# Kernel optimization log

Hardware: AMD Instinct MI355X
Metric: run time of the kernel (lower is better)

The kernel has to match this reference:

```python
import jax, jax.numpy as jnp
import numpy as np

IN_DIM = 128
OUT_DIM = 128
NUM_HEADS = 8
HEAD_DIM = OUT_DIM // NUM_HEADS  # 16
FFN_DIM = OUT_DIM * 2
LN_EPS = 1e-5


def _layer_norm(x, g, b):
    mu = jnp.mean(x, axis=-1, keepdims=True)
    var = jnp.var(x, axis=-1, keepdims=True)
    return (x - mu) * jax.lax.rsqrt(var + LN_EPS) * g + b


def setup_inputs() -> dict:
    key = jax.random.key(0)
    ks = jax.random.split(key, 12)
    B, N = 4, 2048
    s_in = 1.0 / np.sqrt(IN_DIM)
    s_out = 1.0 / np.sqrt(OUT_DIM)
    s_ffn = 1.0 / np.sqrt(FFN_DIM)
    return {
        "adj_matrix": jax.random.randint(ks[0], (N, N), 0, 2, dtype=jnp.int32),
        "h": jax.random.normal(ks[1], (B, N, IN_DIM), dtype=jnp.float32),
        # Q/K/V: Linear(in_dim, out_dim) with use_bias=False, stored as [in, out]
        "Wq": jax.random.uniform(ks[2], (IN_DIM, OUT_DIM), jnp.float32, -s_in, s_in),
        "Wk": jax.random.uniform(ks[3], (IN_DIM, OUT_DIM), jnp.float32, -s_in, s_in),
        "Wv": jax.random.uniform(ks[4], (IN_DIM, OUT_DIM), jnp.float32, -s_in, s_in),
        "Wo": jax.random.uniform(ks[5], (OUT_DIM, OUT_DIM), jnp.float32, -s_out, s_out),
        "bo": jnp.zeros((OUT_DIM,), jnp.float32),
        "ln1_g": jnp.ones((OUT_DIM,), jnp.float32),
        "ln1_b": jnp.zeros((OUT_DIM,), jnp.float32),
        "W1": jax.random.uniform(ks[6], (OUT_DIM, FFN_DIM), jnp.float32, -s_out, s_out),
        "b1": jnp.zeros((FFN_DIM,), jnp.float32),
        "W2": jax.random.uniform(ks[7], (FFN_DIM, OUT_DIM), jnp.float32, -s_ffn, s_ffn),
        "b2": jnp.zeros((OUT_DIM,), jnp.float32),
        "ln2_g": jnp.ones((OUT_DIM,), jnp.float32),
        "ln2_b": jnp.zeros((OUT_DIM,), jnp.float32),
    }


def reference(adj_matrix, h, Wq, Wk, Wv, Wo, bo, ln1_g, ln1_b,
              W1, b1, W2, b2, ln2_g, ln2_b):
    B, N, _ = h.shape
    # QKV projections -> [B, N, H, D]
    Q = (h @ Wq).reshape(B, N, NUM_HEADS, HEAD_DIM)
    K = (h @ Wk).reshape(B, N, NUM_HEADS, HEAD_DIM)
    V = (h @ Wv).reshape(B, N, NUM_HEADS, HEAD_DIM)
    scores = jnp.einsum('bnhd,bmhd->bhnm', Q, K) / jnp.sqrt(
        jnp.asarray(HEAD_DIM, jnp.float32))
    # adjacency-masked attention: mask broadcast over batch and heads
    mask = (adj_matrix == 0)[None, None, :, :]  # [1,1,N,N]
    scores = jnp.where(mask, -jnp.inf, scores)
    attn = jax.nn.softmax(scores, axis=-1)
    attn_out = jnp.einsum('bhnm,bmhd->bnhd', attn, V).reshape(B, N, OUT_DIM)
    # output projection + residual + LN
    x = h + (attn_out @ Wo + bo)
    x = _layer_norm(x, ln1_g, ln1_b)
    # FFN + residual + LN
    y = jax.nn.relu(x @ W1 + b1) @ W2 + b2
    x = _layer_norm(x + y, ln2_g, ln2_b)
    return x
```

## Files before the change

kernel.cpp:

```cpp
#include <hip/hip_runtime.h>

#define B_   4
#define N_   2048
#define DIM  128
#define NH   8
#define HD   16
#define FFN_ 256
#define LN_EPS 1e-5f
#define BN   (B_*N_)
#define LOG2E 1.44269504f

#if __has_builtin(__builtin_amdgcn_exp2f)
#define EXP2(x) __builtin_amdgcn_exp2f(x)
#else
#define EXP2(x) exp2f(x)
#endif

typedef __bf16 bf16x8 __attribute__((ext_vector_type(8)));
typedef short  s16x8  __attribute__((ext_vector_type(8)));
typedef float  f32x16 __attribute__((ext_vector_type(16)));
typedef unsigned int u32x4 __attribute__((ext_vector_type(4)));

template<class T> struct as_short_vec { using type = s16x8; };

template <class T>
__device__ auto mfma_try(T a, T b, f32x16 c, int)
    -> decltype(__builtin_amdgcn_mfma_f32_32x32x16_bf16(a, b, c, 0, 0, 0)) {
  return __builtin_amdgcn_mfma_f32_32x32x16_bf16(a, b, c, 0, 0, 0);
}
template <class T>
__device__ f32x16 mfma_try(T a, T b, f32x16 c, long) {
  return __builtin_amdgcn_mfma_f32_32x32x16_bf16(
      __builtin_bit_cast(typename as_short_vec<T>::type, a),
      __builtin_bit_cast(typename as_short_vec<T>::type, b), c, 0, 0, 0);
}
__device__ __forceinline__ f32x16 mfma_bf(bf16x8 a, bf16x8 b, f32x16 c) {
  return mfma_try(a, b, c, 0);
}

__global__ __launch_bounds__(256) void k_prep(
    const int* __restrict__ adj,
    const float* __restrict__ W1, const float* __restrict__ W2,
    const float* __restrict__ Wq, const float* __restrict__ Wk,
    const float* __restrict__ Wv, const float* __restrict__ Wo,
    unsigned int* __restrict__ adjbT,
    __bf16* __restrict__ W1t, __bf16* __restrict__ W2t,
    __bf16* __restrict__ Wqt, __bf16* __restrict__ Wkt,
    __bf16* __restrict__ Wvt, __bf16* __restrict__ Wot,
    __bf16* __restrict__ onesb) {
    const int blk = blockIdx.x;
    const int tid = threadIdx.x;
    if (blk < 16384) {
        long long idx = (long long)blk * 256 + tid;
        int v = adj[idx] != 0;
        unsigned long long m = __ballot(v);
        if ((tid & 63) == 0) {
            int q  = (int)(idx >> 11);
            int kc = ((int)idx & 2047) >> 5;
            adjbT[(size_t)kc * 2048 + q]       = (unsigned)m;
            adjbT[(size_t)(kc + 1) * 2048 + q] = (unsigned)(m >> 32);
        }
    } else {
        const int g = (blk - 16384) * 256 + tid;
        {
            int k = g >> 8, n = g & 255;
            W1t[(size_t)n * 128 + k] = (__bf16)W1[(size_t)k * 256 + n];
        }
        {
            int k = g >> 7, n = g & 127;
            W2t[(size_t)n * 256 + k] = (__bf16)W2[(size_t)k * 128 + n];
        }
        if (g < 16384) {
            int k = g >> 7, n = g & 127;
            size_t s = (size_t)k * 128 + n, d = (size_t)n * 128 + k;
            Wqt[d] = (__bf16)(Wq[s] * (0.25f * LOG2E));
            Wkt[d] = (__bf16)Wk[s];
            Wvt[d] = (__bf16)Wv[s];
            Wot[d] = (__bf16)Wo[s];
        }
        if (g < 2080) onesb[g] = (__bf16)1.0f;
    }
}

__global__ __launch_bounds__(256) void k_qkv(
    const float* __restrict__ h,
    const __bf16* __restrict__ Wqt, const __bf16* __restrict__ Wkt,
    const __bf16* __restrict__ Wvt,
    __bf16* __restrict__ Qb, __bf16* __restrict__ Kb, __bf16* __restrict__ Vt) {
    const int r0   = blockIdx.x * 32;
    const int tid  = threadIdx.x;
    const int w    = tid >> 6;
    const int lane = tid & 63;
    const int l31  = lane & 31, hi = lane >> 5;

    __shared__ __bf16 Hs[32 * 128];

    for (int i = tid; i < 512; i += 256) {
        int row = i >> 4, u = i & 15;
        const float* src = h + (size_t)(r0 + row) * DIM + u * 8;
        float4 f0 = *(const float4*)src, f1 = *(const float4*)(src + 4);
        bf16x8 v;
        v[0] = (__bf16)f0.x; v[1] = (__bf16)f0.y; v[2] = (__bf16)f0.z; v[3] = (__bf16)f0.w;
        v[4] = (__bf16)f1.x; v[5] = (__bf16)f1.y; v[6] = (__bf16)f1.z; v[7] = (__bf16)f1.w;
        int byte = (row * 256 + u * 16) ^ ((row & 7) << 4);
        *(bf16x8*)((char*)Hs + byte) = v;
    }
    __syncthreads();

    f32x16 aq, ak, av;
    #pragma unroll
    for (int i = 0; i < 16; ++i) { aq[i] = 0.f; ak[i] = 0.f; av[i] = 0.f; }
    #pragma unroll
    for (int kk = 0; kk < 8; ++kk) {
        int byte = (l31 * 256 + kk * 32 + hi * 16) ^ ((l31 & 7) << 4);
        bf16x8 a = *(const bf16x8*)((const char*)Hs + byte);
        const size_t wo = (size_t)(w * 32 + l31) * 128 + kk * 16 + hi * 8;
        aq = mfma_bf(a, *(const bf16x8*)(Wqt + wo), aq);
        ak = mfma_bf(a, *(const bf16x8*)(Wkt + wo), ak);
        av = mfma_bf(a, *(const bf16x8*)(Wvt + wo), av);
    }
    const int n  = w * 32 + l31;
    const int hh = n >> 4, d = n & 15;
    const int b  = r0 >> 11;
    const size_t qbase = (size_t)(b * NH + hh) * N_;
    const size_t vbase = ((size_t)(b * NH + hh) * HD + d) * N_;
    #pragma unroll
    for (int r = 0; r < 16; ++r) {
        int mm   = (r & 3) + 8 * (r >> 2) + 4 * hi;
        int nloc = (r0 & (N_ - 1)) + mm;
        size_t qk = (qbase + nloc) * HD + d;
        Qb[qk] = (__bf16)aq[r];
        Kb[qk] = (__bf16)ak[r];
        int gg = (nloc >> 2) & 7;
        int ng = (gg & 4) | ((gg & 1) << 1) | ((gg >> 1) & 1);
        Vt[vbase + ((nloc & ~31) | (ng << 2) | (nloc & 3))] = (__bf16)av[r];
    }
}

__global__ __launch_bounds__(512, 4) void k_attn(
    const __bf16* __restrict__ Qb, const __bf16* __restrict__ Kb,
    const __bf16* __restrict__ Vt, const unsigned int* __restrict__ adjbT,
    const __bf16* __restrict__ onesb,
    __bf16* __restrict__ AOb) {
    const int bid  = (blockIdx.x & 7) * 256 + (blockIdx.x >> 3);
    const int qt   = bid & 63;
    const int hh   = (bid >> 6) & 7;
    const int b    = bid >> 9;
    const int kq   = threadIdx.x >> 6;
    const int lane = threadIdx.x & 63;
    const int l31  = lane & 31, hi = lane >> 5;
    const int q     = qt * 32 + l31;
    const int kbase = kq * 256;
    const int NT    = 8;

    __shared__ float accL[7][64][9];
    __shared__ uint2 lutM[16];

    if (threadIdx.x < 16) {
        unsigned v = threadIdx.x;
        lutM[v].x = ((v & 1u) ? 0xFFFFu : 0u) | ((v & 2u) ? 0xFFFF0000u : 0u);
        lutM[v].y = ((v & 4u) ? 0xFFFFu : 0u) | ((v & 8u) ? 0xFFFF0000u : 0u);
    }
    __syncthreads();

    const __bf16* Qh = Qb + (size_t)(b * NH + hh) * N_ * HD;
    const __bf16* Kp = Kb + (size_t)(b * NH + hh) * N_ * HD
                          + (size_t)(kbase + l31) * HD + hi * 8;
    const __bf16* Vp = ((l31 < 16)
        ? (Vt + ((size_t)(b * NH + hh) * HD + l31) * N_)
        : onesb) + kbase + hi * 8;
    const unsigned int* wp = adjbT + (size_t)(kq * NT) * 2048 + q;

    bf16x8 qf = *(const bf16x8*)(Qh + (size_t)q * HD + hi * 8);

    f32x16 acc;
    #pragma unroll
    for (int i = 0; i < 16; ++i) acc[i] = 0.f;
    const f32x16 z = {};

    bf16x8 kf  = *(const bf16x8*)Kp;
    bf16x8 vfa = *(const bf16x8*)Vp;
    bf16x8 vfb = *(const bf16x8*)(Vp + 16);
    unsigned int w32 = wp[0];

    #pragma unroll
    for (int t = 0; t < NT; ++t) {
        bf16x8 kf_n = {}, vfa_n = {}, vfb_n = {};
        unsigned int w32_n = 0;
        if (t + 1 < NT) {
            kf_n  = *(const bf16x8*)(Kp + (t + 1) * 32 * HD);
            vfa_n = *(const bf16x8*)(Vp + (t + 1) * 32);
            vfb_n = *(const bf16x8*)(Vp + (t + 1) * 32 + 16);
            w32_n = wp[(size_t)(t + 1) * 2048];
        }

        const unsigned ws = w32 >> (4 * hi);
        uint2 e0 = lutM[ws & 15u];
        uint2 e1 = lutM[(ws >> 8) & 15u];
        uint2 e2 = lutM[(ws >> 16) & 15u];
        uint2 e3 = lutM[(ws >> 24) & 15u];

        f32x16 st = mfma_bf(kf, qf, z);

        float p[16];
        #pragma unroll
        for (int r = 0; r < 16; ++r) p[r] = EXP2(st[r]);
        bf16x8 pa, pb;
        #pragma unroll
        for (int r = 0; r < 8; ++r) { pa[r] = (__bf16)p[r]; pb[r] = (__bf16)p[r + 8]; }

        u32x4 mA = {e0.x, e0.y, e1.x, e1.y};
        u32x4 mB = {e2.x, e2.y, e3.x, e3.y};
        pa = __builtin_bit_cast(bf16x8, __builtin_bit_cast(u32x4, pa) & mA);
        pb = __builtin_bit_cast(bf16x8, __builtin_bit_cast(u32x4, pb) & mB);

        acc = mfma_bf(vfa, pa, acc);
        acc = mfma_bf(vfb, pb, acc);

        if (t + 1 < NT) { kf = kf_n; vfa = vfa_n; vfb = vfb_n; w32 = w32_n; }
    }

    if (kq != 0) {
        #pragma unroll
        for (int r = 0; r < 9; ++r) accL[kq - 1][lane][r] = acc[r];
    }
    __syncthreads();
    if (kq == 0) {
        float tot[9];
        #pragma unroll
        for (int r = 0; r < 9; ++r) {
            float v = acc[r];
            #pragma unroll
            for (int i = 0; i < 7; ++i) v += accL[i][lane][r];
            tot[r] = v;
        }
        float inv = 1.f / tot[8];
        bf16x8 ov;
        #pragma unroll
        for (int r = 0; r < 8; ++r) ov[r] = (__bf16)(tot[r] * inv);
        u32x4 ou = __builtin_bit_cast(u32x4, ov);
        __bf16* op = AOb + ((size_t)(b * N_ + q)) * DIM + hh * HD + 4 * hi;
        uint2 w0 = { ou[0], ou[1] }, w1 = { ou[2], ou[3] };
        *(uint2*)op       = w0;
        *(uint2*)(op + 8) = w1;
    }
}

__global__ __launch_bounds__(256) void k_tail(
    const __bf16* __restrict__ AOb, const float* __restrict__ h,
    const __bf16* __restrict__ Wot, const float* __restrict__ bo,
    const float* __restrict__ g1, const float* __restrict__ b1ln,
    const __bf16* __restrict__ W1t, const float* __restrict__ b1,
    const __bf16* __restrict__ W2t, const float* __restrict__ b2,
    const float* __restrict__ g2, const float* __restrict__ b2ln,
    float* __restrict__ out) {
    const int r0   = blockIdx.x * 32;
    const int tid  = threadIdx.x;
    const int w    = tid >> 6;
    const int lane = tid & 63;
    const int l31  = lane & 31, hi = lane >> 5;

    __shared__ __bf16 As[32 * 128];
    __shared__ __bf16 Xs[32 * 128];
    __shared__ __bf16 Ts[32 * 256];
    __shared__ float  vv[32][DIM];

    for (int i = tid; i < 512; i += 256) {
        int row = i >> 4, u = i & 15;
        bf16x8 v = *(const bf16x8*)(AOb + (size_t)(r0 + row) * DIM + u * 8);
        int byte = (row * 256 + u * 16) ^ ((row & 7) << 4);
        *(bf16x8*)((char*)As + byte) = v;
    }
    __syncthreads();

    f32x16 acc;
    #pragma unroll
    for (int i = 0; i < 16; ++i) acc[i] = 0.f;
    #pragma unroll
    for (int kk = 0; kk < 8; ++kk) {
        int byte = (l31 * 256 + kk * 32 + hi * 16) ^ ((l31 & 7) << 4);
        bf16x8 a = *(const bf16x8*)((const char*)As + byte);
        acc = mfma_bf(a, *(const bf16x8*)(Wot + (size_t)(w * 32 + l31) * 128 + kk * 16 + hi * 8), acc);
    }
    {
        int n = w * 32 + l31;
        float bb = bo[n];
        #pragma unroll
        for (int r = 0; r < 16; ++r) {
            int mm = (r & 3) + 8 * (r >> 2) + 4 * hi;
            vv[mm][n] = acc[r] + bb + h[(size_t)(r0 + mm) * DIM + n];
        }
    }
    __syncthreads();

    {
        const int ln = lane;
        float gc0 = g1[ln], bc0 = b1ln[ln], gc1 = g1[ln + 64], bc1 = b1ln[ln + 64];
        #pragma unroll
        for (int i = 0; i < 8; ++i) {
            int rr = w * 8 + i;
            float x0 = vv[rr][ln], x1 = vv[rr][ln + 64];
            float s = x0 + x1, s2 = x0 * x0 + x1 * x1;
            for (int off = 1; off < 64; off <<= 1) {
                s  += __shfl_xor(s,  off);
                s2 += __shfl_xor(s2, off);
            }
            float mu  = s * (1.f / DIM);
            float var = s2 * (1.f / DIM) - mu * mu;
            float rs  = rsqrtf(var + LN_EPS);
            int byte0 = (rr * 256 + ln * 2) ^ ((rr & 7) << 4);
            int byte1 = (rr * 256 + (ln + 64) * 2) ^ ((rr & 7) << 4);
            *(__bf16*)((char*)Xs + byte0) = (__bf16)((x0 - mu) * rs * gc0 + bc0);
            *(__bf16*)((char*)Xs + byte1) = (__bf16)((x1 - mu) * rs * gc1 + bc1);
        }
    }
    __syncthreads();

    f32x16 acc1a, acc1b;
    #pragma unroll
    for (int i = 0; i < 16; ++i) { acc1a[i] = 0.f; acc1b[i] = 0.f; }
    #pragma unroll
    for (int kk = 0; kk < 8; ++kk) {
        int byte = (l31 * 256 + kk * 32 + hi * 16) ^ ((l31 & 7) << 4);
        bf16x8 a = *(const bf16x8*)((const char*)Xs + byte);
        bf16x8 bA = *(const bf16x8*)(W1t + (size_t)(w * 32 + l31) * 128 + kk * 16 + hi * 8);
        bf16x8 bB = *(const bf16x8*)(W1t + (size_t)((w + 4) * 32 + l31) * 128 + kk * 16 + hi * 8);
        acc1a = mfma_bf(a, bA, acc1a);
        acc1b = mfma_bf(a, bB, acc1b);
    }
    #pragma unroll
    for (int ct = 0; ct < 2; ++ct) {
        const f32x16& ac = ct ? acc1b : acc1a;
        int n = (w + ct * 4) * 32 + l31;
        float bb = b1[n];
        #pragma unroll
        for (int r = 0; r < 16; ++r) {
            int mm = (r & 3) + 8 * (r >> 2) + 4 * hi;
            float v = fmaxf(ac[r] + bb, 0.f);
            int byte = (mm * 512 + n * 2) ^ ((mm & 7) << 4);
            *(__bf16*)((char*)Ts + byte) = (__bf16)v;
        }
    }
    __syncthreads();

    f32x16 acc2;
    #pragma unroll
    for (int i = 0; i < 16; ++i) acc2[i] = 0.f;
    #pragma unroll
    for (int kk = 0; kk < 16; ++kk) {
        int byte = (l31 * 512 + kk * 32 + hi * 16) ^ ((l31 & 7) << 4);
        bf16x8 a = *(const bf16x8*)((const char*)Ts + byte);
        bf16x8 bb = *(const bf16x8*)(W2t + (size_t)(w * 32 + l31) * 256 + kk * 16 + hi * 8);
        acc2 = mfma_bf(a, bb, acc2);
    }
    {
        int n = w * 32 + l31;
        float bb = b2[n];
        #pragma unroll
        for (int r = 0; r < 16; ++r) {
            int mm = (r & 3) + 8 * (r >> 2) + 4 * hi;
            int byteR = (mm * 256 + n * 2) ^ ((mm & 7) << 4);
            float resid = (float)*(const __bf16*)((const char*)Xs + byteR);
            vv[mm][n] = acc2[r] + bb + resid;
        }
    }
    __syncthreads();

    {
        const int ln = lane;
        float gc0 = g2[ln], bc0 = b2ln[ln], gc1 = g2[ln + 64], bc1 = b2ln[ln + 64];
        #pragma unroll
        for (int i = 0; i < 8; ++i) {
            int rr = w * 8 + i;
            float x0 = vv[rr][ln], x1 = vv[rr][ln + 64];
            float s = x0 + x1, s2 = x0 * x0 + x1 * x1;
            for (int off = 1; off < 64; off <<= 1) {
                s  += __shfl_xor(s,  off);
                s2 += __shfl_xor(s2, off);
            }
            float mu  = s * (1.f / DIM);
            float var = s2 * (1.f / DIM) - mu * mu;
            float rs  = rsqrtf(var + LN_EPS);
            size_t o = (size_t)(r0 + rr) * DIM;
            out[o + ln]      = (x0 - mu) * rs * gc0 + bc0;
            out[o + ln + 64] = (x1 - mu) * rs * gc1 + bc1;
        }
    }
}

extern "C" void kernel_launch(void* const* d_in, const int* in_sizes, int n_in,
                              void* d_out, int out_size, void* d_ws, size_t ws_size,
                              hipStream_t stream) {
    const int*   adj = (const int*)  d_in[0];
    const float* h   = (const float*)d_in[1];
    const float* Wq  = (const float*)d_in[2];
    const float* Wk  = (const float*)d_in[3];
    const float* Wv  = (const float*)d_in[4];
    const float* Wo  = (const float*)d_in[5];
    const float* bo  = (const float*)d_in[6];
    const float* g1  = (const float*)d_in[7];
    const float* b1l = (const float*)d_in[8];
    const float* W1  = (const float*)d_in[9];
    const float* b1  = (const float*)d_in[10];
    const float* W2  = (const float*)d_in[11];
    const float* b2  = (const float*)d_in[12];
    const float* g2  = (const float*)d_in[13];
    const float* b2l = (const float*)d_in[14];
    float* out = (float*)d_out;

    __bf16* AOb = (__bf16*)d_ws;
    unsigned int* adjbT = (unsigned int*)(AOb + (size_t)BN * DIM);
    __bf16* Qb  = (__bf16*)(adjbT + (size_t)64 * 2048);
    __bf16* Kb  = Qb + (size_t)BN * DIM;
    __bf16* Vt  = Kb + (size_t)BN * DIM;
    __bf16* W1t = Vt + (size_t)BN * DIM;
    __bf16* W2t = W1t + (size_t)DIM * FFN_;
    __bf16* Wqt = W2t + (size_t)DIM * FFN_;
    __bf16* Wkt = Wqt + (size_t)DIM * DIM;
    __bf16* Wvt = Wkt + (size_t)DIM * DIM;
    __bf16* Wot = Wvt + (size_t)DIM * DIM;
    __bf16* onesb = Wot + (size_t)DIM * DIM;

    hipLaunchKernelGGL(k_prep, dim3(16384 + 128), dim3(256), 0, stream,
                       adj, W1, W2, Wq, Wk, Wv, Wo,
                       adjbT, W1t, W2t, Wqt, Wkt, Wvt, Wot, onesb);
    hipLaunchKernelGGL(k_qkv, dim3(BN / 32), dim3(256), 0, stream,
                       h, Wqt, Wkt, Wvt, Qb, Kb, Vt);
    hipLaunchKernelGGL(k_attn, dim3(B_ * NH * (N_ / 32)), dim3(512), 0, stream,
                       Qb, Kb, Vt, adjbT, onesb, AOb);
    hipLaunchKernelGGL(k_tail, dim3(BN / 32), dim3(256), 0, stream,
                       AOb, h, Wot, bo, g1, b1l, W1t, b1, W2t, b2, g2, b2l, out);
}
```

Before: 60.01 us.

## Stage QKV outputs in LDS for coalesced stores; prefetch FFN weights to registers

The QKV kernel now writes its MFMA results into padded shared-memory tiles and then issues 16-byte vector stores to global Q, K and the permuted transposed V. Previously each element went out as a scattered 2-byte store. The FFN kernel also loads its Wo and W1 weight fragments into registers at the start, so those global loads overlap with staging the input tile. The cost is more LDS use, an extra barrier, and about 96 more VGPRs of weights, which may reduce occupancy.

```diff
diff --git a/kernel.cpp b/kernel.cpp
--- a/kernel.cpp
+++ b/kernel.cpp
@@ -94,6 +94,9 @@
     const int l31  = lane & 31, hi = lane >> 5;
 
     __shared__ __bf16 Hs[32 * 128];
+    __shared__ __bf16 Qs[32 * 136];
+    __shared__ __bf16 Ks[32 * 136];
+    __shared__ __bf16 Vs[128 * 40];
 
     for (int i = tid; i < 512; i += 256) {
         int row = i >> 4, u = i & 15;
@@ -119,21 +122,39 @@
         ak = mfma_bf(a, *(const bf16x8*)(Wkt + wo), ak);
         av = mfma_bf(a, *(const bf16x8*)(Wvt + wo), av);
     }
-    const int n  = w * 32 + l31;
-    const int hh = n >> 4, d = n & 15;
-    const int b  = r0 >> 11;
-    const size_t qbase = (size_t)(b * NH + hh) * N_;
-    const size_t vbase = ((size_t)(b * NH + hh) * HD + d) * N_;
+
+    const int n = w * 32 + l31;
     #pragma unroll
     for (int r = 0; r < 16; ++r) {
-        int mm   = (r & 3) + 8 * (r >> 2) + 4 * hi;
-        int nloc = (r0 & (N_ - 1)) + mm;
-        size_t qk = (qbase + nloc) * HD + d;
-        Qb[qk] = (__bf16)aq[r];
-        Kb[qk] = (__bf16)ak[r];
-        int gg = (nloc >> 2) & 7;
-        int ng = (gg & 4) | ((gg & 1) << 1) | ((gg >> 1) & 1);
-        Vt[vbase + ((nloc & ~31) | (ng << 2) | (nloc & 3))] = (__bf16)av[r];
+        int mm = (r & 3) + 8 * (r >> 2) + 4 * hi;
+        Qs[mm * 136 + n] = (__bf16)aq[r];
+        Ks[mm * 136 + n] = (__bf16)ak[r];
+        int g  = (mm >> 2) & 7;
+        int ng = (g & 4) | ((g & 1) << 1) | ((g >> 1) & 1);
+        int p  = (ng << 2) | (mm & 3);
+        Vs[n * 40 + p] = (__bf16)av[r];
+    }
+    __syncthreads();
+
+    const int b = r0 >> 11;
+    const int nloc0 = r0 & (N_ - 1);
+    {
+        int row = tid & 31, hh = tid >> 5;
+        size_t dst = ((size_t)(b * NH + hh) * N_ + nloc0 + row) * HD;
+        const __bf16* sq = Qs + row * 136 + hh * 16;
+        const __bf16* sk = Ks + row * 136 + hh * 16;
+        *(bf16x8*)(Qb + dst)     = *(const bf16x8*)sq;
+        *(bf16x8*)(Qb + dst + 8) = *(const bf16x8*)(sq + 8);
+        *(bf16x8*)(Kb + dst)     = *(const bf16x8*)sk;
+        *(bf16x8*)(Kb + dst + 8) = *(const bf16x8*)(sk + 8);
+    }
+    {
+        int nn = tid >> 1, half = tid & 1;
+        int hh = nn >> 4, d = nn & 15;
+        size_t dst = ((size_t)(b * NH + hh) * HD + d) * N_ + nloc0 + half * 16;
+        const __bf16* sv = Vs + nn * 40 + half * 16;
+        *(bf16x8*)(Vt + dst)     = *(const bf16x8*)sv;
+        *(bf16x8*)(Vt + dst + 8) = *(const bf16x8*)(sv + 8);
     }
 }
 
@@ -265,6 +286,15 @@
     __shared__ __bf16 Ts[32 * 256];
     __shared__ float  vv[32][DIM];
 
+    bf16x8 wo_f[8], w1a_f[8], w1b_f[8];
+    #pragma unroll
+    for (int kk = 0; kk < 8; ++kk) {
+        const size_t o = (size_t)(w * 32 + l31) * 128 + kk * 16 + hi * 8;
+        wo_f[kk]  = *(const bf16x8*)(Wot + o);
+        w1a_f[kk] = *(const bf16x8*)(W1t + o);
+        w1b_f[kk] = *(const bf16x8*)(W1t + (size_t)128 * 128 + o);
+    }
+
     for (int i = tid; i < 512; i += 256) {
         int row = i >> 4, u = i & 15;
         bf16x8 v = *(const bf16x8*)(AOb + (size_t)(r0 + row) * DIM + u * 8);
@@ -280,7 +310,7 @@
     for (int kk = 0; kk < 8; ++kk) {
         int byte = (l31 * 256 + kk * 32 + hi * 16) ^ ((l31 & 7) << 4);
         bf16x8 a = *(const bf16x8*)((const char*)As + byte);
-        acc = mfma_bf(a, *(const bf16x8*)(Wot + (size_t)(w * 32 + l31) * 128 + kk * 16 + hi * 8), acc);
+        acc = mfma_bf(a, wo_f[kk], acc);
     }
     {
         int n = w * 32 + l31;
@@ -323,10 +353,8 @@
     for (int kk = 0; kk < 8; ++kk) {
         int byte = (l31 * 256 + kk * 32 + hi * 16) ^ ((l31 & 7) << 4);
         bf16x8 a = *(const bf16x8*)((const char*)Xs + byte);
-        bf16x8 bA = *(const bf16x8*)(W1t + (size_t)(w * 32 + l31) * 128 + kk * 16 + hi * 8);
-        bf16x8 bB = *(const bf16x8*)(W1t + (size_t)((w + 4) * 32 + l31) * 128 + kk * 16 + hi * 8);
-        acc1a = mfma_bf(a, bA, acc1a);
-        acc1b = mfma_bf(a, bB, acc1b);
+        acc1a = mfma_bf(a, w1a_f[kk], acc1a);
+        acc1b = mfma_bf(a, w1b_f[kk], acc1b);
     }
     #pragma unroll
     for (int ct = 0; ct < 2; ++ct) {
```

New measurement: 63.73 us. 1.06x slower.

## Spread QKV and tail GEMM work across more waves per block

Applied to the files above, without the earlier changes.

k_qkv now launches 768 threads so each of 12 waves computes one 32-column tile of a single Q, K or V matrix, where before each of 4 waves handled all three. k_tail uses 512 threads: the Wo and W2 GEMMs split K across two wave groups and reduce the partials through a new shared-memory buffer, and W1 gives each wave one column tile. The aim is more waves in flight and less serial MFMA work per wave in these small GEMM kernels. In exchange it adds extra shared memory, extra syncs and reduction traffic, and larger blocks may lower occupancy.

```diff
diff --git a/kernel.cpp b/kernel.cpp
--- a/kernel.cpp
+++ b/kernel.cpp
@@ -82,7 +82,7 @@
     }
 }
 
-__global__ __launch_bounds__(256) void k_qkv(
+__global__ __launch_bounds__(768) void k_qkv(
     const float* __restrict__ h,
     const __bf16* __restrict__ Wqt, const __bf16* __restrict__ Wkt,
     const __bf16* __restrict__ Wvt,
@@ -90,13 +90,15 @@
     const int r0   = blockIdx.x * 32;
     const int tid  = threadIdx.x;
     const int w    = tid >> 6;
+    const int mat  = w >> 2;
+    const int ct   = w & 3;
     const int lane = tid & 63;
     const int l31  = lane & 31, hi = lane >> 5;
 
     __shared__ __bf16 Hs[32 * 128];
 
-    for (int i = tid; i < 512; i += 256) {
-        int row = i >> 4, u = i & 15;
+    if (tid < 512) {
+        int row = tid >> 4, u = tid & 15;
         const float* src = h + (size_t)(r0 + row) * DIM + u * 8;
         float4 f0 = *(const float4*)src, f1 = *(const float4*)(src + 4);
         bf16x8 v;
@@ -107,33 +109,40 @@
     }
     __syncthreads();
 
-    f32x16 aq, ak, av;
-    #pragma unroll
-    for (int i = 0; i < 16; ++i) { aq[i] = 0.f; ak[i] = 0.f; av[i] = 0.f; }
+    const __bf16* Wsel = (mat == 0) ? Wqt : ((mat == 1) ? Wkt : Wvt);
+
+    f32x16 a;
+    #pragma unroll
+    for (int i = 0; i < 16; ++i) a[i] = 0.f;
     #pragma unroll
     for (int kk = 0; kk < 8; ++kk) {
         int byte = (l31 * 256 + kk * 32 + hi * 16) ^ ((l31 & 7) << 4);
-        bf16x8 a = *(const bf16x8*)((const char*)Hs + byte);
-        const size_t wo = (size_t)(w * 32 + l31) * 128 + kk * 16 + hi * 8;
-        aq = mfma_bf(a, *(const bf16x8*)(Wqt + wo), aq);
-        ak = mfma_bf(a, *(const bf16x8*)(Wkt + wo), ak);
-        av = mfma_bf(a, *(const bf16x8*)(Wvt + wo), av);
-    }
-    const int n  = w * 32 + l31;
+        bf16x8 af = *(const bf16x8*)((const char*)Hs + byte);
+        a = mfma_bf(af, *(const bf16x8*)(Wsel + (size_t)(ct * 32 + l31) * 128 + kk * 16 + hi * 8), a);
+    }
+
+    const int n  = ct * 32 + l31;
     const int hh = n >> 4, d = n & 15;
     const int b  = r0 >> 11;
-    const size_t qbase = (size_t)(b * NH + hh) * N_;
-    const size_t vbase = ((size_t)(b * NH + hh) * HD + d) * N_;
-    #pragma unroll
-    for (int r = 0; r < 16; ++r) {
-        int mm   = (r & 3) + 8 * (r >> 2) + 4 * hi;
-        int nloc = (r0 & (N_ - 1)) + mm;
-        size_t qk = (qbase + nloc) * HD + d;
-        Qb[qk] = (__bf16)aq[r];
-        Kb[qk] = (__bf16)ak[r];
-        int gg = (nloc >> 2) & 7;
-        int ng = (gg & 4) | ((gg & 1) << 1) | ((gg >> 1) & 1);
-        Vt[vbase + ((nloc & ~31) | (ng << 2) | (nloc & 3))] = (__bf16)av[r];
+    const int nloc0 = r0 & (N_ - 1);
+    if (mat < 2) {
+        __bf16* dst = (mat == 0) ? Qb : Kb;
+        const size_t qbase = (size_t)(b * NH + hh) * N_;
+        #pragma unroll
+        for (int r = 0; r < 16; ++r) {
+            int mm = (r & 3) + 8 * (r >> 2) + 4 * hi;
+            dst[(qbase + nloc0 + mm) * HD + d] = (__bf16)a[r];
+        }
+    } else {
+        const size_t vbase = ((size_t)(b * NH + hh) * HD + d) * N_;
+        #pragma unroll
+        for (int r = 0; r < 16; ++r) {
+            int mm   = (r & 3) + 8 * (r >> 2) + 4 * hi;
+            int nloc = nloc0 + mm;
+            int gg = (nloc >> 2) & 7;
+            int ng = (gg & 4) | ((gg & 1) << 1) | ((gg >> 1) & 1);
+            Vt[vbase + ((nloc & ~31) | (ng << 2) | (nloc & 3))] = (__bf16)a[r];
+        }
     }
 }
 
@@ -246,7 +255,7 @@
     }
 }
 
-__global__ __launch_bounds__(256) void k_tail(
+__global__ __launch_bounds__(512) void k_tail(
     const __bf16* __restrict__ AOb, const float* __restrict__ h,
     const __bf16* __restrict__ Wot, const float* __restrict__ bo,
     const float* __restrict__ g1, const float* __restrict__ b1ln,
@@ -257,6 +266,8 @@
     const int r0   = blockIdx.x * 32;
     const int tid  = threadIdx.x;
     const int w    = tid >> 6;
+    const int ct   = w & 3;
+    const int kh   = w >> 2;
     const int lane = tid & 63;
     const int l31  = lane & 31, hi = lane >> 5;
 
@@ -264,9 +275,10 @@
     __shared__ __bf16 Xs[32 * 128];
     __shared__ __bf16 Ts[32 * 256];
     __shared__ float  vv[32][DIM];
-
-    for (int i = tid; i < 512; i += 256) {
-        int row = i >> 4, u = i & 15;
+    __shared__ float  accT[4][64][16];
+
+    {
+        int row = tid >> 4, u = tid & 15;
         bf16x8 v = *(const bf16x8*)(AOb + (size_t)(r0 + row) * DIM + u * 8);
         int byte = (row * 256 + u * 16) ^ ((row & 7) << 4);
         *(bf16x8*)((char*)As + byte) = v;
@@ -277,18 +289,24 @@
     #pragma unroll
     for (int i = 0; i < 16; ++i) acc[i] = 0.f;
     #pragma unroll
-    for (int kk = 0; kk < 8; ++kk) {
-        int byte = (l31 * 256 + kk * 32 + hi * 16) ^ ((l31 & 7) << 4);
+    for (int kk = 0; kk < 4; ++kk) {
+        int kkk = kh * 4 + kk;
+        int byte = (l31 * 256 + kkk * 32 + hi * 16) ^ ((l31 & 7) << 4);
         bf16x8 a = *(const bf16x8*)((const char*)As + byte);
-        acc = mfma_bf(a, *(const bf16x8*)(Wot + (size_t)(w * 32 + l31) * 128 + kk * 16 + hi * 8), acc);
-    }
-    {
-        int n = w * 32 + l31;
+        acc = mfma_bf(a, *(const bf16x8*)(Wot + (size_t)(ct * 32 + l31) * 128 + kkk * 16 + hi * 8), acc);
+    }
+    if (kh == 1) {
+        #pragma unroll
+        for (int r = 0; r < 16; ++r) accT[ct][lane][r] = acc[r];
+    }
+    __syncthreads();
+    if (kh == 0) {
+        int n = ct * 32 + l31;
         float bb = bo[n];
         #pragma unroll
         for (int r = 0; r < 16; ++r) {
             int mm = (r & 3) + 8 * (r >> 2) + 4 * hi;
-            vv[mm][n] = acc[r] + bb + h[(size_t)(r0 + mm) * DIM + n];
+            vv[mm][n] = acc[r] + accT[ct][lane][r] + bb + h[(size_t)(r0 + mm) * DIM + n];
         }
     }
     __syncthreads();
@@ -297,8 +315,8 @@
         const int ln = lane;
         float gc0 = g1[ln], bc0 = b1ln[ln], gc1 = g1[ln + 64], bc1 = b1ln[ln + 64];
         #pragma unroll
-        for (int i = 0; i < 8; ++i) {
-            int rr = w * 8 + i;
+        for (int i = 0; i < 4; ++i) {
+            int rr = w * 4 + i;
             float x0 = vv[rr][ln], x1 = vv[rr][ln + 64];
             float s = x0 + x1, s2 = x0 * x0 + x1 * x1;
             for (int off = 1; off < 64; off <<= 1) {
@@ -316,27 +334,22 @@
     }
     __syncthreads();
 
-    f32x16 acc1a, acc1b;
-    #pragma unroll
-    for (int i = 0; i < 16; ++i) { acc1a[i] = 0.f; acc1b[i] = 0.f; }
+    f32x16 acc1;
+    #pragma unroll
+    for (int i = 0; i < 16; ++i) acc1[i] = 0.f;
     #pragma unroll
     for (int kk = 0; kk < 8; ++kk) {
         int byte = (l31 * 256 + kk * 32 + hi * 16) ^ ((l31 & 7) << 4);
         bf16x8 a = *(const bf16x8*)((const char*)Xs + byte);
-        bf16x8 bA = *(const bf16x8*)(W1t + (size_t)(w * 32 + l31) * 128 + kk * 16 + hi * 8);
-        bf16x8 bB = *(const bf16x8*)(W1t + (size_t)((w + 4) * 32 + l31) * 128 + kk * 16 + hi * 8);
-        acc1a = mfma_bf(a, bA, acc1a);
-        acc1b = mfma_bf(a, bB, acc1b);
-    }
-    #pragma unroll
-    for (int ct = 0; ct < 2; ++ct) {
-        const f32x16& ac = ct ? acc1b : acc1a;
-        int n = (w + ct * 4) * 32 + l31;
+        acc1 = mfma_bf(a, *(const bf16x8*)(W1t + (size_t)(w * 32 + l31) * 128 + kk * 16 + hi * 8), acc1);
+    }
+    {
+        int n = w * 32 + l31;
         float bb = b1[n];
         #pragma unroll
         for (int r = 0; r < 16; ++r) {
             int mm = (r & 3) + 8 * (r >> 2) + 4 * hi;
-            float v = fmaxf(ac[r] + bb, 0.f);
+            float v = fmaxf(acc1[r] + bb, 0.f);
             int byte = (mm * 512 + n * 2) ^ ((mm & 7) << 4);
             *(__bf16*)((char*)Ts + byte) = (__bf16)v;
         }
@@ -347,21 +360,26 @@
     #pragma unroll
     for (int i = 0; i < 16; ++i) acc2[i] = 0.f;
     #pragma unroll
-    for (int kk = 0; kk < 16; ++kk) {
-        int byte = (l31 * 512 + kk * 32 + hi * 16) ^ ((l31 & 7) << 4);
+    for (int kk = 0; kk < 8; ++kk) {
+        int kkk = kh * 8 + kk;
+        int byte = (l31 * 512 + kkk * 32 + hi * 16) ^ ((l31 & 7) << 4);
         bf16x8 a = *(const bf16x8*)((const char*)Ts + byte);
-        bf16x8 bb = *(const bf16x8*)(W2t + (size_t)(w * 32 + l31) * 256 + kk * 16 + hi * 8);
-        acc2 = mfma_bf(a, bb, acc2);
-    }
-    {
-        int n = w * 32 + l31;
+        acc2 = mfma_bf(a, *(const bf16x8*)(W2t + (size_t)(ct * 32 + l31) * 256 + kkk * 16 + hi * 8), acc2);
+    }
+    if (kh == 1) {
+        #pragma unroll
+        for (int r = 0; r < 16; ++r) accT[ct][lane][r] = acc2[r];
+    }
+    __syncthreads();
+    if (kh == 0) {
+        int n = ct * 32 + l31;
         float bb = b2[n];
         #pragma unroll
         for (int r = 0; r < 16; ++r) {
             int mm = (r & 3) + 8 * (r >> 2) + 4 * hi;
             int byteR = (mm * 256 + n * 2) ^ ((mm & 7) << 4);
             float resid = (float)*(const __bf16*)((const char*)Xs + byteR);
-            vv[mm][n] = acc2[r] + bb + resid;
+            vv[mm][n] = acc2[r] + accT[ct][lane][r] + bb + resid;
         }
     }
     __syncthreads();
@@ -370,8 +388,8 @@
         const int ln = lane;
         float gc0 = g2[ln], bc0 = b2ln[ln], gc1 = g2[ln + 64], bc1 = b2ln[ln + 64];
         #pragma unroll
-        for (int i = 0; i < 8; ++i) {
-            int rr = w * 8 + i;
+        for (int i = 0; i < 4; ++i) {
+            int rr = w * 4 + i;
             float x0 = vv[rr][ln], x1 = vv[rr][ln + 64];
             float s = x0 + x1, s2 = x0 * x0 + x1 * x1;
             for (int off = 1; off < 64; off <<= 1) {
@@ -424,10 +442,10 @@
     hipLaunchKernelGGL(k_prep, dim3(16384 + 128), dim3(256), 0, stream,
                        adj, W1, W2, Wq, Wk, Wv, Wo,
                        adjbT, W1t, W2t, Wqt, Wkt, Wvt, Wot, onesb);
-    hipLaunchKernelGGL(k_qkv, dim3(BN / 32), dim3(256), 0, stream,
+    hipLaunchKernelGGL(k_qkv, dim3(BN / 32), dim3(768), 0, stream,
                        h, Wqt, Wkt, Wvt, Qb, Kb, Vt);
     hipLaunchKernelGGL(k_attn, dim3(B_ * NH * (N_ / 32)), dim3(512), 0, stream,
                        Qb, Kb, Vt, adjbT, onesb, AOb);
-    hipLaunchKernelGGL(k_tail, dim3(BN / 32), dim3(256), 0, stream,
+    hipLaunchKernelGGL(k_tail, dim3(BN / 32), dim3(512), 0, stream,
                        AOb, h, Wot, bo, g1, b1l, W1t, b1, W2t, b2, g2, b2l, out);
 }
```

After: 58.12 us (median of 2 runs). 1.03x faster.
